# Kernel optimization log

Hardware: AMD Instinct MI355X
Metric: run time of the kernel (lower is better)

## Reference

```python
import jax, jax.numpy as jnp
import numpy as np

DIM = 768
HEADS = 12
HIDDEN = 3072
EPS = 1e-5  # torch nn.LayerNorm default


def _layer_norm(x, w, b):
    m = jnp.mean(x, axis=-1, keepdims=True)
    v = jnp.mean(jnp.square(x - m), axis=-1, keepdims=True)
    return (x - m) * jax.lax.rsqrt(v + EPS) * w + b


def setup_inputs() -> dict:
    key = jax.random.key(0)
    ks = jax.random.split(key, 10)
    s = lambda fan_in: 1.0 / np.sqrt(fan_in)
    return {
        "x": jax.random.normal(ks[0], (4, 2048, DIM), dtype=jnp.float32),
        "ln1_w": jnp.ones((DIM,), jnp.float32),
        "ln1_b": jnp.zeros((DIM,), jnp.float32),
        "qkv_w": jax.random.normal(ks[1], (3 * DIM, DIM), jnp.float32) * s(DIM),
        "qkv_b": jnp.zeros((3 * DIM,), jnp.float32),
        "proj_w": jax.random.normal(ks[2], (DIM, DIM), jnp.float32) * s(DIM),
        "proj_b": jnp.zeros((DIM,), jnp.float32),
        "ln2_w": jnp.ones((DIM,), jnp.float32),
        "ln2_b": jnp.zeros((DIM,), jnp.float32),
        "fc1_w": jax.random.normal(ks[3], (HIDDEN, DIM), jnp.float32) * s(DIM),
        "fc1_b": jnp.zeros((HIDDEN,), jnp.float32),
        "fc2_w": jax.random.normal(ks[4], (DIM, HIDDEN), jnp.float32) * s(HIDDEN),
        "fc2_b": jnp.zeros((DIM,), jnp.float32),
    }


def _attention(x, qkv_w, qkv_b, proj_w, proj_b):
    B, N, C = x.shape
    H = HEADS
    D = C // H
    scale = D ** -0.5
    qkv = x @ qkv_w.T + qkv_b                       # [B,N,3C]
    qkv = qkv.reshape(B, N, 3, H, D)
    q, k, v = jnp.moveaxis(qkv, 2, 0)               # each [B,N,H,D]
    attn = jnp.einsum("bnhd,bmhd->bhnm", q, k) * scale
    attn = jax.nn.softmax(attn, axis=-1)
    out = jnp.einsum("bhnm,bmhd->bnhd", attn, v).reshape(B, N, C)
    return out @ proj_w.T + proj_b


def reference(x, ln1_w, ln1_b, qkv_w, qkv_b, proj_w, proj_b,
              ln2_w, ln2_b, fc1_w, fc1_b, fc2_w, fc2_b):
    x = x + _attention(_layer_norm(x, ln1_w, ln1_b), qkv_w, qkv_b, proj_w, proj_b)
    h = _layer_norm(x, ln2_w, ln2_b)
    h = jax.nn.gelu(h @ fc1_w.T + fc1_b, approximate=False)
    x = x + (h @ fc2_w.T + fc2_b)
    return x
```

## Files before the change

kernel.cpp:

```cpp
#include <hip/hip_runtime.h>
#include <cstddef>


typedef _Float16 h8 __attribute__((ext_vector_type(8)));
typedef _Float16 h4 __attribute__((ext_vector_type(4)));
typedef _Float16 h2 __attribute__((ext_vector_type(2)));
typedef float f4 __attribute__((ext_vector_type(4)));

#define MFMA16(a, b, c) __builtin_amdgcn_mfma_f32_16x16x32_f16((a), (b), (c), 0, 0, 0)

__device__ __forceinline__ _Float16 f2h(float x) { return (_Float16)x; }
__device__ __forceinline__ h2 pk2(float a, float b) {
    return __builtin_bit_cast(h2, __builtin_amdgcn_cvt_pkrtz(a, b));
}
__device__ __forceinline__ h4 pk4(float a, float b, float c, float d) {
    h2 p0 = pk2(a, b);
    h2 p1 = pk2(c, d);
    h4 r; r[0] = p0[0]; r[1] = p0[1]; r[2] = p1[0]; r[3] = p1[1];
    return r;
}

__device__ __forceinline__ void gl_lds16(const _Float16* g, _Float16* l) {
    __builtin_amdgcn_global_load_lds(
        (const __attribute__((address_space(1))) void*)g,
        (__attribute__((address_space(3))) void*)l, 16, 0, 0);
}

__global__ void cvt_all(const float* __restrict__ s0, _Float16* __restrict__ d0, int n0,
                        const float* __restrict__ s1, _Float16* __restrict__ d1, int n1,
                        const float* __restrict__ s2, _Float16* __restrict__ d2, int n2,
                        const float* __restrict__ s3, _Float16* __restrict__ d3) {
    int i = (blockIdx.x * 256 + threadIdx.x) * 4;
    const float* s; _Float16* d; int base;
    if (i < n0) { s = s0; d = d0; base = 0; }
    else if (i < n0 + n1) { s = s1; d = d1; base = n0; }
    else if (i < n0 + n1 + n2) { s = s2; d = d2; base = n0 + n1; }
    else { s = s3; d = d3; base = n0 + n1 + n2; }
    int j = i - base;
    float4 v = *(const float4*)(s + j);
    *(h4*)(d + j) = pk4(v.x, v.y, v.z, v.w);
}

__global__ void ln_f16(const float* __restrict__ x, const float* __restrict__ w,
                       const float* __restrict__ b, _Float16* __restrict__ out) {
    int row = blockIdx.x;
    int tid = threadIdx.x;
    float4 v = ((const float4*)(x + (size_t)row * 768))[tid];
    float s = v.x + v.y + v.z + v.w;
    float s2 = v.x * v.x + v.y * v.y + v.z * v.z + v.w * v.w;
#pragma unroll
    for (int off = 32; off > 0; off >>= 1) {
        s += __shfl_down(s, off, 64);
        s2 += __shfl_down(s2, off, 64);
    }
    __shared__ float red[6];
    if ((tid & 63) == 0) { red[tid >> 6] = s; red[3 + (tid >> 6)] = s2; }
    __syncthreads();
    s = red[0] + red[1] + red[2];
    s2 = red[3] + red[4] + red[5];
    float mean = s * (1.0f / 768.0f);
    float rstd = rsqrtf(s2 * (1.0f / 768.0f) - mean * mean + 1e-5f);
    float4 wv = ((const float4*)w)[tid];
    float4 bv = ((const float4*)b)[tid];
    *(h4*)(out + (size_t)row * 768 + tid * 4) =
        pk4((v.x - mean) * rstd * wv.x + bv.x, (v.y - mean) * rstd * wv.y + bv.y,
            (v.z - mean) * rstd * wv.z + bv.z, (v.w - mean) * rstd * wv.w + bv.w);
}

enum { MODE_QKV = 0, MODE_PROJ = 1, MODE_FC1 = 2, MODE_FC2 = 3 };

template <int MODE, int TM>
__global__ __launch_bounds__(256, TM == 64 ? 4 : 3) void gemm_bt(
    const _Float16* __restrict__ A, const _Float16* __restrict__ W,
    const float* __restrict__ bias, const float* __restrict__ resid,
    float* __restrict__ outF, _Float16* __restrict__ oq,
    _Float16* __restrict__ okk, _Float16* __restrict__ ov, int K) {
    constexpr int MI = TM / 32;
    constexpr int AI = TM / 32;
    __shared__ _Float16 As[TM * 64];
    __shared__ _Float16 Bs[128 * 64];
    int bm = blockIdx.x * TM, bn = blockIdx.y * 128;
    int tid = threadIdx.x;
    int wave = tid >> 6, lane = tid & 63, quad = lane >> 4, l15 = lane & 15;
    int wrow = (wave >> 1) * (TM / 2), wcol = (wave & 1) * 64;
    int lr = lane >> 3;
    int sw = ((lane & 7) ^ lr) * 8;
    int rsw = (l15 & 7) * 8;
    f4 acc[MI][4];
#pragma unroll
    for (int mi = 0; mi < MI; mi++)
#pragma unroll
        for (int ni = 0; ni < 4; ni++) acc[mi][ni] = (f4){0.f, 0.f, 0.f, 0.f};

    const _Float16* ApG[AI];
    _Float16* AsL[AI];
#pragma unroll
    for (int i = 0; i < AI; i++) {
        int r = wave * (TM / 4) + i * 8;
        ApG[i] = A + (size_t)(bm + r + lr) * K + sw;
        AsL[i] = As + r * 64;
    }
    const _Float16* WpG[4];
    _Float16* BsL[4];
#pragma unroll
    for (int i = 0; i < 4; i++) {
        int r = wave * 32 + i * 8;
        WpG[i] = W + (size_t)(bn + r + lr) * K + sw;
        BsL[i] = Bs + r * 64;
    }

    for (int k0 = 0; k0 < K; k0 += 64) {
        __syncthreads();
#pragma unroll
        for (int i = 0; i < AI; i++) { gl_lds16(ApG[i], AsL[i]); ApG[i] += 64; }
#pragma unroll
        for (int i = 0; i < 4; i++) { gl_lds16(WpG[i], BsL[i]); WpG[i] += 64; }
        __syncthreads();
#pragma unroll
        for (int ks = 0; ks < 2; ks++) {
            h8 af[MI], bfr[4];
#pragma unroll
            for (int mi = 0; mi < MI; mi++)
                af[mi] = *(const h8*)&As[(wrow + 16 * mi + l15) * 64 +
                                         (((4 * ks + quad) * 8) ^ rsw)];
#pragma unroll
            for (int ni = 0; ni < 4; ni++)
                bfr[ni] = *(const h8*)&Bs[(wcol + 16 * ni + l15) * 64 +
                                          (((4 * ks + quad) * 8) ^ rsw)];
#pragma unroll
            for (int mi = 0; mi < MI; mi++)
#pragma unroll
                for (int ni = 0; ni < 4; ni++)
                    acc[mi][ni] = MFMA16(af[mi], bfr[ni], acc[mi][ni]);
        }
    }

#pragma unroll
    for (int mi = 0; mi < MI; mi++) {
#pragma unroll
        for (int ni = 0; ni < 4; ni++) {
            int col = bn + wcol + 16 * ni + l15;
            float bc = bias[col];
            int m0 = bm + wrow + 16 * mi + quad * 4;
            float v0 = acc[mi][ni][0] + bc, v1 = acc[mi][ni][1] + bc;
            float v2 = acc[mi][ni][2] + bc, v3 = acc[mi][ni][3] + bc;
            if (MODE == MODE_QKV) {
                int sec = col / 768;
                int rem = col - sec * 768;
                int h = rem >> 6, d = rem & 63;
                int b_ = m0 >> 11, ns = m0 & 2047;
                size_t bh = (size_t)(b_ * 12 + h);
                if (sec == 0) {
                    size_t base = (bh * 2048 + ns) * 64 + d;
                    oq[base] = f2h(v0 * 0.18033688f);
                    oq[base + 64] = f2h(v1 * 0.18033688f);
                    oq[base + 128] = f2h(v2 * 0.18033688f);
                    oq[base + 192] = f2h(v3 * 0.18033688f);
                } else if (sec == 1) {
                    size_t base = (bh * 2048 + ns) * 64 + d;
                    okk[base] = f2h(v0);
                    okk[base + 64] = f2h(v1);
                    okk[base + 128] = f2h(v2);
                    okk[base + 192] = f2h(v3);
                } else {
                    *(h4*)&ov[(bh * 64 + d) * 2048 + ns] = pk4(v0, v1, v2, v3);
                }
            } else if (MODE == MODE_FC1) {
                float g0 = __expf(v0 * (1.5957691f + 0.14295405f * v0 * v0));
                float g1 = __expf(v1 * (1.5957691f + 0.14295405f * v1 * v1));
                float g2 = __expf(v2 * (1.5957691f + 0.14295405f * v2 * v2));
                float g3 = __expf(v3 * (1.5957691f + 0.14295405f * v3 * v3));
                size_t base = (size_t)m0 * 3072 + col;
                oq[base] = f2h(v0 * g0 / (1.f + g0));
                oq[base + 3072] = f2h(v1 * g1 / (1.f + g1));
                oq[base + 6144] = f2h(v2 * g2 / (1.f + g2));
                oq[base + 9216] = f2h(v3 * g3 / (1.f + g3));
            } else {
                size_t idx = (size_t)m0 * 768 + col;
                outF[idx] = v0 + resid[idx];
                outF[idx + 768] = v1 + resid[idx + 768];
                outF[idx + 1536] = v2 + resid[idx + 1536];
                outF[idx + 2304] = v3 + resid[idx + 2304];
            }
        }
    }
}

__global__ __launch_bounds__(256, 4) void attn_kernel(
    const _Float16* __restrict__ Q, const _Float16* __restrict__ Kp,
    const _Float16* __restrict__ Vt, _Float16* __restrict__ O0p,
    _Float16* __restrict__ O1p, float* __restrict__ Lp) {
    int qt = blockIdx.x;
    int bh = blockIdx.y;
    int sp = blockIdx.z;
    int tid = threadIdx.x;
    int wave = tid >> 6, lane = tid & 63, quad = lane >> 4, l15 = lane & 15;
    int lr = lane >> 3;
    int sw = ((lane & 7) ^ lr) * 8;
    int rsw = (l15 & 7) * 8;

    __shared__ _Float16 Ks[64 * 64];
    __shared__ _Float16 Vs[64 * 64];
    __shared__ _Float16 Ps[4][32 * 64];

    h8 qf[2][2];
    {
        const _Float16* Qb =
            Q + (((size_t)bh * 2048) + qt * 128 + wave * 32 + l15) * 64 + quad * 8;
#pragma unroll
        for (int qc = 0; qc < 2; qc++)
#pragma unroll
            for (int ks = 0; ks < 2; ks++)
                qf[qc][ks] = *(const h8*)(Qb + qc * 16 * 64 + ks * 32);
    }
    h8 onesv;
#pragma unroll
    for (int j = 0; j < 8; j++) onesv[j] = (_Float16)1.0f;

    f4 Oa[4][2];
    f4 Ls[2];
#pragma unroll
    for (int dc = 0; dc < 4; dc++)
#pragma unroll
        for (int qc = 0; qc < 2; qc++) Oa[dc][qc] = (f4){0.f, 0.f, 0.f, 0.f};
    Ls[0] = (f4){0.f, 0.f, 0.f, 0.f};
    Ls[1] = (f4){0.f, 0.f, 0.f, 0.f};

    const _Float16* Kg = Kp + (size_t)bh * 2048 * 64;
    const _Float16* Vg = Vt + (size_t)bh * 64 * 2048;
    const _Float16* KpG[2];
    const _Float16* VpG[2];
    _Float16* KsL[2];
    _Float16* VsL[2];
#pragma unroll
    for (int i = 0; i < 2; i++) {
        int r = wave * 16 + i * 8;
        KpG[i] = Kg + (size_t)(sp * 1024 + r + lr) * 64 + sw;
        VpG[i] = Vg + (size_t)(r + lr) * 2048 + sp * 1024 + sw;
        KsL[i] = Ks + r * 64;
        VsL[i] = Vs + r * 64;
    }
    _Float16* PsW = Ps[wave];

    for (int it = 0; it < 16; it++) {
        __syncthreads();
#pragma unroll
        for (int i = 0; i < 2; i++) {
            gl_lds16(KpG[i], KsL[i]); KpG[i] += 4096;
            gl_lds16(VpG[i], VsL[i]); VpG[i] += 64;
        }
        __syncthreads();

        f4 Sa[4][2];
#pragma unroll
        for (int kc = 0; kc < 4; kc++)
#pragma unroll
            for (int qc = 0; qc < 2; qc++) Sa[kc][qc] = (f4){0.f, 0.f, 0.f, 0.f};
#pragma unroll
        for (int ks = 0; ks < 2; ks++) {
            h8 kf[4];
#pragma unroll
            for (int kc = 0; kc < 4; kc++)
                kf[kc] = *(const h8*)&Ks[(16 * kc + l15) * 64 +
                                         (((4 * ks + quad) * 8) ^ rsw)];
#pragma unroll
            for (int kc = 0; kc < 4; kc++)
#pragma unroll
                for (int qc = 0; qc < 2; qc++)
                    Sa[kc][qc] = MFMA16(kf[kc], qf[qc][ks], Sa[kc][qc]);
        }

#pragma unroll
        for (int kc = 0; kc < 4; kc++) {
#pragma unroll
            for (int qc = 0; qc < 2; qc++) {
                h4 p = pk4(exp2f(Sa[kc][qc][0]), exp2f(Sa[kc][qc][1]),
                           exp2f(Sa[kc][qc][2]), exp2f(Sa[kc][qc][3]));
                *(h4*)&PsW[(16 * qc + l15) * 64 + (((2 * kc + (quad >> 1)) * 8) ^ rsw) +
                           (quad & 1) * 4] = p;
            }
        }

#pragma unroll
        for (int ks = 0; ks < 2; ks++) {
            h8 vf[4], pf[2];
#pragma unroll
            for (int dc = 0; dc < 4; dc++)
                vf[dc] = *(const h8*)&Vs[(16 * dc + l15) * 64 +
                                         (((4 * ks + quad) * 8) ^ rsw)];
#pragma unroll
            for (int qc = 0; qc < 2; qc++)
                pf[qc] = *(const h8*)&PsW[(16 * qc + l15) * 64 +
                                          (((4 * ks + quad) * 8) ^ rsw)];
#pragma unroll
            for (int dc = 0; dc < 4; dc++)
#pragma unroll
                for (int qc = 0; qc < 2; qc++)
                    Oa[dc][qc] = MFMA16(vf[dc], pf[qc], Oa[dc][qc]);
#pragma unroll
            for (int qc = 0; qc < 2; qc++)
                Ls[qc] = MFMA16(onesv, pf[qc], Ls[qc]);
        }
    }

    _Float16* Op = (sp == 0 ? O0p : O1p);
#pragma unroll
    for (int qc = 0; qc < 2; qc++) {
        int n = qt * 128 + wave * 32 + 16 * qc + l15;
        size_t rbase = ((size_t)bh * 2048 + n) * 64;
#pragma unroll
        for (int dc = 0; dc < 4; dc++) {
            f4 o = Oa[dc][qc];
            *(h4*)&Op[rbase + 16 * dc + quad * 4] =
                pk4(o[0] * 0.015625f, o[1] * 0.015625f, o[2] * 0.015625f, o[3] * 0.015625f);
        }
        if (quad == 0) Lp[(size_t)sp * 98304 + (size_t)bh * 2048 + n] = Ls[qc][0];
    }
}

__global__ void attn_combine(const _Float16* __restrict__ O0p,
                             const _Float16* __restrict__ O1p,
                             const float* __restrict__ Lp,
                             _Float16* __restrict__ O) {
    int gid = blockIdx.x * 256 + threadIdx.x;
    int idx = gid >> 4;
    int dg = (gid & 15) * 4;
    int bh = idx >> 11, n = idx & 2047;
    size_t pbase = (size_t)idx * 64 + dg;
    h4 a = *(const h4*)&O0p[pbase];
    h4 b = *(const h4*)&O1p[pbase];
    float inv = 64.0f / (Lp[idx] + Lp[98304 + idx]);
    int b_ = bh / 12, h = bh - b_ * 12;
    *(h4*)&O[((size_t)b_ * 2048 + n) * 768 + h * 64 + dg] =
        pk4(((float)a[0] + (float)b[0]) * inv, ((float)a[1] + (float)b[1]) * inv,
            ((float)a[2] + (float)b[2]) * inv, ((float)a[3] + (float)b[3]) * inv);
}

extern "C" void kernel_launch(void* const* d_in, const int* in_sizes, int n_in,
                              void* d_out, int out_size, void* d_ws, size_t ws_size,
                              hipStream_t stream) {
    const float* x      = (const float*)d_in[0];
    const float* ln1_w  = (const float*)d_in[1];
    const float* ln1_b  = (const float*)d_in[2];
    const float* qkv_w  = (const float*)d_in[3];
    const float* qkv_b  = (const float*)d_in[4];
    const float* proj_w = (const float*)d_in[5];
    const float* proj_b = (const float*)d_in[6];
    const float* ln2_w  = (const float*)d_in[7];
    const float* ln2_b  = (const float*)d_in[8];
    const float* fc1_w  = (const float*)d_in[9];
    const float* fc1_b  = (const float*)d_in[10];
    const float* fc2_w  = (const float*)d_in[11];
    const float* fc2_b  = (const float*)d_in[12];
    float* out = (float*)d_out;

    char* ws = (char*)d_ws;
    size_t off = 0;
    _Float16* wqkv  = (_Float16*)(ws + off); off += (size_t)2304 * 768 * 2;
    _Float16* wproj = (_Float16*)(ws + off); off += (size_t)768 * 768 * 2;
    _Float16* wfc1  = (_Float16*)(ws + off); off += (size_t)3072 * 768 * 2;
    _Float16* wfc2  = (_Float16*)(ws + off); off += (size_t)768 * 3072 * 2;
    _Float16* actA  = (_Float16*)(ws + off); off += (size_t)8192 * 768 * 2;
    _Float16* big   = (_Float16*)(ws + off); off += (size_t)8192 * 3072 * 2;
    _Float16* O0p   = (_Float16*)(ws + off); off += (size_t)48 * 2048 * 64 * 2;
    float*    Lp    = (float*)(ws + off);    off += (size_t)2 * 48 * 2048 * 4;
    _Float16* qb = big;
    _Float16* kb = big + (size_t)48 * 2048 * 64;
    _Float16* vb = big + (size_t)2 * 48 * 2048 * 64;
    _Float16* O1p = big + (size_t)3 * 48 * 2048 * 64;
    _Float16* hb = big;

    cvt_all<<<6912, 256, 0, stream>>>(qkv_w, wqkv, 2304 * 768, proj_w, wproj, 768 * 768,
                                      fc1_w, wfc1, 3072 * 768, fc2_w, wfc2);

    ln_f16<<<8192, 192, 0, stream>>>(x, ln1_w, ln1_b, actA);
    gemm_bt<MODE_QKV, 128><<<dim3(64, 18), 256, 0, stream>>>(actA, wqkv, qkv_b, nullptr,
                                                             nullptr, qb, kb, vb, 768);
    attn_kernel<<<dim3(16, 48, 2), 256, 0, stream>>>(qb, kb, vb, O0p, O1p, Lp);
    attn_combine<<<6144, 256, 0, stream>>>(O0p, O1p, Lp, actA);
    gemm_bt<MODE_PROJ, 64><<<dim3(128, 6), 256, 0, stream>>>(actA, wproj, proj_b, x, out,
                                                             nullptr, nullptr, nullptr, 768);
    ln_f16<<<8192, 192, 0, stream>>>(out, ln2_w, ln2_b, actA);
    gemm_bt<MODE_FC1, 128><<<dim3(64, 24), 256, 0, stream>>>(actA, wfc1, fc1_b, nullptr,
                                                             nullptr, hb, nullptr, nullptr, 768);
    gemm_bt<MODE_FC2, 64><<<dim3(128, 6), 256, 0, stream>>>(hb, wfc2, fc2_b, out, out,
                                                            nullptr, nullptr, nullptr, 3072);
}
```

Measured before the change: 382.6 us.

## Double-buffer GEMM and attention LDS tiles, drop attention split-K combine

Makes the GEMM and attention kernels double-buffer their LDS tiles, so the next K/V or A/W tile is fetched while the current one is consumed, and removes one barrier per iteration. All GEMMs now use 64-row tiles. The attention kernel no longer splits the key range in two: each block walks all 32 key tiles, normalizes by its own row sum, and writes straight into the [B,N,C] layout, which removes the combine kernel and its partial buffers. The cost is more LDS per block, lower occupancy (launch bounds drop to 3) and fewer attention blocks in flight.

```diff
diff --git a/kernel.cpp b/kernel.cpp
--- a/kernel.cpp
+++ b/kernel.cpp
@@ -69,66 +69,70 @@
 
 enum { MODE_QKV = 0, MODE_PROJ = 1, MODE_FC1 = 2, MODE_FC2 = 3 };
 
-template <int MODE, int TM>
-__global__ __launch_bounds__(256, TM == 64 ? 4 : 3) void gemm_bt(
+template <int MODE>
+__global__ __launch_bounds__(256, 3) void gemm_bt(
     const _Float16* __restrict__ A, const _Float16* __restrict__ W,
     const float* __restrict__ bias, const float* __restrict__ resid,
     float* __restrict__ outF, _Float16* __restrict__ oq,
     _Float16* __restrict__ okk, _Float16* __restrict__ ov, int K) {
-    constexpr int MI = TM / 32;
-    constexpr int AI = TM / 32;
-    __shared__ _Float16 As[TM * 64];
-    __shared__ _Float16 Bs[128 * 64];
-    int bm = blockIdx.x * TM, bn = blockIdx.y * 128;
+    __shared__ _Float16 As[2 * 64 * 64];
+    __shared__ _Float16 Bs[2 * 128 * 64];
+    int bm = blockIdx.x * 64, bn = blockIdx.y * 128;
     int tid = threadIdx.x;
     int wave = tid >> 6, lane = tid & 63, quad = lane >> 4, l15 = lane & 15;
-    int wrow = (wave >> 1) * (TM / 2), wcol = (wave & 1) * 64;
+    int wrow = (wave >> 1) * 32, wcol = (wave & 1) * 64;
     int lr = lane >> 3;
     int sw = ((lane & 7) ^ lr) * 8;
     int rsw = (l15 & 7) * 8;
-    f4 acc[MI][4];
-#pragma unroll
-    for (int mi = 0; mi < MI; mi++)
+    f4 acc[2][4];
+#pragma unroll
+    for (int mi = 0; mi < 2; mi++)
 #pragma unroll
         for (int ni = 0; ni < 4; ni++) acc[mi][ni] = (f4){0.f, 0.f, 0.f, 0.f};
 
-    const _Float16* ApG[AI];
-    _Float16* AsL[AI];
-#pragma unroll
-    for (int i = 0; i < AI; i++) {
-        int r = wave * (TM / 4) + i * 8;
-        ApG[i] = A + (size_t)(bm + r + lr) * K + sw;
-        AsL[i] = As + r * 64;
+    const _Float16* ApG[2];
+    int rA[2];
+#pragma unroll
+    for (int i = 0; i < 2; i++) {
+        rA[i] = wave * 16 + i * 8;
+        ApG[i] = A + (size_t)(bm + rA[i] + lr) * K + sw;
     }
     const _Float16* WpG[4];
-    _Float16* BsL[4];
+    int rB[4];
 #pragma unroll
     for (int i = 0; i < 4; i++) {
-        int r = wave * 32 + i * 8;
-        WpG[i] = W + (size_t)(bn + r + lr) * K + sw;
-        BsL[i] = Bs + r * 64;
-    }
-
-    for (int k0 = 0; k0 < K; k0 += 64) {
+        rB[i] = wave * 32 + i * 8;
+        WpG[i] = W + (size_t)(bn + rB[i] + lr) * K + sw;
+    }
+
+#pragma unroll
+    for (int i = 0; i < 2; i++) { gl_lds16(ApG[i], As + rA[i] * 64); ApG[i] += 64; }
+#pragma unroll
+    for (int i = 0; i < 4; i++) { gl_lds16(WpG[i], Bs + rB[i] * 64); WpG[i] += 64; }
+
+    int nIter = K >> 6;
+    for (int it = 0; it < nIter; it++) {
+        int bufA = (it & 1) * 4096, bufN = ((it & 1) ^ 1) * 4096;
         __syncthreads();
-#pragma unroll
-        for (int i = 0; i < AI; i++) { gl_lds16(ApG[i], AsL[i]); ApG[i] += 64; }
-#pragma unroll
-        for (int i = 0; i < 4; i++) { gl_lds16(WpG[i], BsL[i]); WpG[i] += 64; }
-        __syncthreads();
+        if (it + 1 < nIter) {
+#pragma unroll
+            for (int i = 0; i < 2; i++) { gl_lds16(ApG[i], As + bufN + rA[i] * 64); ApG[i] += 64; }
+#pragma unroll
+            for (int i = 0; i < 4; i++) { gl_lds16(WpG[i], Bs + 2 * bufN + rB[i] * 64); WpG[i] += 64; }
+        }
 #pragma unroll
         for (int ks = 0; ks < 2; ks++) {
-            h8 af[MI], bfr[4];
-#pragma unroll
-            for (int mi = 0; mi < MI; mi++)
-                af[mi] = *(const h8*)&As[(wrow + 16 * mi + l15) * 64 +
+            h8 af[2], bfr[4];
+#pragma unroll
+            for (int mi = 0; mi < 2; mi++)
+                af[mi] = *(const h8*)&As[bufA + (wrow + 16 * mi + l15) * 64 +
                                          (((4 * ks + quad) * 8) ^ rsw)];
 #pragma unroll
             for (int ni = 0; ni < 4; ni++)
-                bfr[ni] = *(const h8*)&Bs[(wcol + 16 * ni + l15) * 64 +
+                bfr[ni] = *(const h8*)&Bs[2 * bufA + (wcol + 16 * ni + l15) * 64 +
                                           (((4 * ks + quad) * 8) ^ rsw)];
 #pragma unroll
-            for (int mi = 0; mi < MI; mi++)
+            for (int mi = 0; mi < 2; mi++)
 #pragma unroll
                 for (int ni = 0; ni < 4; ni++)
                     acc[mi][ni] = MFMA16(af[mi], bfr[ni], acc[mi][ni]);
@@ -136,7 +140,7 @@
     }
 
 #pragma unroll
-    for (int mi = 0; mi < MI; mi++) {
+    for (int mi = 0; mi < 2; mi++) {
 #pragma unroll
         for (int ni = 0; ni < 4; ni++) {
             int col = bn + wcol + 16 * ni + l15;
@@ -186,21 +190,19 @@
     }
 }
 
-__global__ __launch_bounds__(256, 4) void attn_kernel(
+__global__ __launch_bounds__(256, 3) void attn_kernel(
     const _Float16* __restrict__ Q, const _Float16* __restrict__ Kp,
-    const _Float16* __restrict__ Vt, _Float16* __restrict__ O0p,
-    _Float16* __restrict__ O1p, float* __restrict__ Lp) {
-    int qt = blockIdx.x;
-    int bh = blockIdx.y;
-    int sp = blockIdx.z;
+    const _Float16* __restrict__ Vt, _Float16* __restrict__ O) {
+    int bh = blockIdx.x;
+    int qt = blockIdx.y;
     int tid = threadIdx.x;
     int wave = tid >> 6, lane = tid & 63, quad = lane >> 4, l15 = lane & 15;
     int lr = lane >> 3;
     int sw = ((lane & 7) ^ lr) * 8;
     int rsw = (l15 & 7) * 8;
 
-    __shared__ _Float16 Ks[64 * 64];
-    __shared__ _Float16 Vs[64 * 64];
+    __shared__ _Float16 Ks[2 * 64 * 64];
+    __shared__ _Float16 Vs[2 * 64 * 64];
     __shared__ _Float16 Ps[4][32 * 64];
 
     h8 qf[2][2];
@@ -230,26 +232,31 @@
     const _Float16* Vg = Vt + (size_t)bh * 64 * 2048;
     const _Float16* KpG[2];
     const _Float16* VpG[2];
-    _Float16* KsL[2];
-    _Float16* VsL[2];
+    int rKV[2];
 #pragma unroll
     for (int i = 0; i < 2; i++) {
-        int r = wave * 16 + i * 8;
-        KpG[i] = Kg + (size_t)(sp * 1024 + r + lr) * 64 + sw;
-        VpG[i] = Vg + (size_t)(r + lr) * 2048 + sp * 1024 + sw;
-        KsL[i] = Ks + r * 64;
-        VsL[i] = Vs + r * 64;
+        rKV[i] = wave * 16 + i * 8;
+        KpG[i] = Kg + (size_t)(rKV[i] + lr) * 64 + sw;
+        VpG[i] = Vg + (size_t)(rKV[i] + lr) * 2048 + sw;
     }
     _Float16* PsW = Ps[wave];
 
-    for (int it = 0; it < 16; it++) {
+#pragma unroll
+    for (int i = 0; i < 2; i++) {
+        gl_lds16(KpG[i], Ks + rKV[i] * 64); KpG[i] += 4096;
+        gl_lds16(VpG[i], Vs + rKV[i] * 64); VpG[i] += 64;
+    }
+
+    for (int it = 0; it < 32; it++) {
+        int bufC = (it & 1) * 4096, bufN = ((it & 1) ^ 1) * 4096;
         __syncthreads();
-#pragma unroll
-        for (int i = 0; i < 2; i++) {
-            gl_lds16(KpG[i], KsL[i]); KpG[i] += 4096;
-            gl_lds16(VpG[i], VsL[i]); VpG[i] += 64;
-        }
-        __syncthreads();
+        if (it + 1 < 32) {
+#pragma unroll
+            for (int i = 0; i < 2; i++) {
+                gl_lds16(KpG[i], Ks + bufN + rKV[i] * 64); KpG[i] += 4096;
+                gl_lds16(VpG[i], Vs + bufN + rKV[i] * 64); VpG[i] += 64;
+            }
+        }
 
         f4 Sa[4][2];
 #pragma unroll
@@ -261,7 +268,7 @@
             h8 kf[4];
 #pragma unroll
             for (int kc = 0; kc < 4; kc++)
-                kf[kc] = *(const h8*)&Ks[(16 * kc + l15) * 64 +
+                kf[kc] = *(const h8*)&Ks[bufC + (16 * kc + l15) * 64 +
                                          (((4 * ks + quad) * 8) ^ rsw)];
 #pragma unroll
             for (int kc = 0; kc < 4; kc++)
@@ -286,7 +293,7 @@
             h8 vf[4], pf[2];
 #pragma unroll
             for (int dc = 0; dc < 4; dc++)
-                vf[dc] = *(const h8*)&Vs[(16 * dc + l15) * 64 +
+                vf[dc] = *(const h8*)&Vs[bufC + (16 * dc + l15) * 64 +
                                          (((4 * ks + quad) * 8) ^ rsw)];
 #pragma unroll
             for (int qc = 0; qc < 2; qc++)
@@ -303,37 +310,19 @@
         }
     }
 
-    _Float16* Op = (sp == 0 ? O0p : O1p);
+    int b_ = bh / 12, h = bh - b_ * 12;
 #pragma unroll
     for (int qc = 0; qc < 2; qc++) {
+        float inv = 1.0f / Ls[qc][0];
         int n = qt * 128 + wave * 32 + 16 * qc + l15;
-        size_t rbase = ((size_t)bh * 2048 + n) * 64;
+        size_t base = ((size_t)b_ * 2048 + n) * 768 + h * 64;
 #pragma unroll
         for (int dc = 0; dc < 4; dc++) {
             f4 o = Oa[dc][qc];
-            *(h4*)&Op[rbase + 16 * dc + quad * 4] =
-                pk4(o[0] * 0.015625f, o[1] * 0.015625f, o[2] * 0.015625f, o[3] * 0.015625f);
-        }
-        if (quad == 0) Lp[(size_t)sp * 98304 + (size_t)bh * 2048 + n] = Ls[qc][0];
-    }
-}
-
-__global__ void attn_combine(const _Float16* __restrict__ O0p,
-                             const _Float16* __restrict__ O1p,
-                             const float* __restrict__ Lp,
-                             _Float16* __restrict__ O) {
-    int gid = blockIdx.x * 256 + threadIdx.x;
-    int idx = gid >> 4;
-    int dg = (gid & 15) * 4;
-    int bh = idx >> 11, n = idx & 2047;
-    size_t pbase = (size_t)idx * 64 + dg;
-    h4 a = *(const h4*)&O0p[pbase];
-    h4 b = *(const h4*)&O1p[pbase];
-    float inv = 64.0f / (Lp[idx] + Lp[98304 + idx]);
-    int b_ = bh / 12, h = bh - b_ * 12;
-    *(h4*)&O[((size_t)b_ * 2048 + n) * 768 + h * 64 + dg] =
-        pk4(((float)a[0] + (float)b[0]) * inv, ((float)a[1] + (float)b[1]) * inv,
-            ((float)a[2] + (float)b[2]) * inv, ((float)a[3] + (float)b[3]) * inv);
+            *(h4*)&O[base + 16 * dc + quad * 4] =
+                pk4(o[0] * inv, o[1] * inv, o[2] * inv, o[3] * inv);
+        }
+    }
 }
 
 extern "C" void kernel_launch(void* const* d_in, const int* in_sizes, int n_in,
@@ -362,27 +351,23 @@
     _Float16* wfc2  = (_Float16*)(ws + off); off += (size_t)768 * 3072 * 2;
     _Float16* actA  = (_Float16*)(ws + off); off += (size_t)8192 * 768 * 2;
     _Float16* big   = (_Float16*)(ws + off); off += (size_t)8192 * 3072 * 2;
-    _Float16* O0p   = (_Float16*)(ws + off); off += (size_t)48 * 2048 * 64 * 2;
-    float*    Lp    = (float*)(ws + off);    off += (size_t)2 * 48 * 2048 * 4;
     _Float16* qb = big;
     _Float16* kb = big + (size_t)48 * 2048 * 64;
     _Float16* vb = big + (size_t)2 * 48 * 2048 * 64;
-    _Float16* O1p = big + (size_t)3 * 48 * 2048 * 64;
     _Float16* hb = big;
 
     cvt_all<<<6912, 256, 0, stream>>>(qkv_w, wqkv, 2304 * 768, proj_w, wproj, 768 * 768,
                                       fc1_w, wfc1, 3072 * 768, fc2_w, wfc2);
 
     ln_f16<<<8192, 192, 0, stream>>>(x, ln1_w, ln1_b, actA);
-    gemm_bt<MODE_QKV, 128><<<dim3(64, 18), 256, 0, stream>>>(actA, wqkv, qkv_b, nullptr,
-                                                             nullptr, qb, kb, vb, 768);
-    attn_kernel<<<dim3(16, 48, 2), 256, 0, stream>>>(qb, kb, vb, O0p, O1p, Lp);
-    attn_combine<<<6144, 256, 0, stream>>>(O0p, O1p, Lp, actA);
-    gemm_bt<MODE_PROJ, 64><<<dim3(128, 6), 256, 0, stream>>>(actA, wproj, proj_b, x, out,
-                                                             nullptr, nullptr, nullptr, 768);
+    gemm_bt<MODE_QKV><<<dim3(128, 18), 256, 0, stream>>>(actA, wqkv, qkv_b, nullptr,
+                                                         nullptr, qb, kb, vb, 768);
+    attn_kernel<<<dim3(48, 16), 256, 0, stream>>>(qb, kb, vb, actA);
+    gemm_bt<MODE_PROJ><<<dim3(128, 6), 256, 0, stream>>>(actA, wproj, proj_b, x, out,
+                                                         nullptr, nullptr, nullptr, 768);
     ln_f16<<<8192, 192, 0, stream>>>(out, ln2_w, ln2_b, actA);
-    gemm_bt<MODE_FC1, 128><<<dim3(64, 24), 256, 0, stream>>>(actA, wfc1, fc1_b, nullptr,
-                                                             nullptr, hb, nullptr, nullptr, 768);
-    gemm_bt<MODE_FC2, 64><<<dim3(128, 6), 256, 0, stream>>>(hb, wfc2, fc2_b, out, out,
-                                                            nullptr, nullptr, nullptr, 3072);
-}
+    gemm_bt<MODE_FC1><<<dim3(128, 24), 256, 0, stream>>>(actA, wfc1, fc1_b, nullptr,
+                                                         nullptr, hb, nullptr, nullptr, 768);
+    gemm_bt<MODE_FC2><<<dim3(128, 6), 256, 0, stream>>>(hb, wfc2, fc2_b, out, out,
+                                                        nullptr, nullptr, nullptr, 3072);
+}
```

After: 379.5 us. Within noise of the previous version (-0.8%).

## Drop attention split-K, double-buffer K/V tiles, keep P in registers

Applied to the files above, without the earlier changes.

The attention kernel no longer splits the key range across two blocks. Each block now walks all 32 K/V tiles and normalizes its output directly, so the combine kernel and the partial-output buffers go away. K/V loads are double-buffered so the next tile's global-to-LDS copy overlaps compute, removing one barrier per iteration. The P matrix stays in registers and feeds 16x16x16 MFMAs instead of round-tripping through LDS. In exchange the grid has half as many blocks, the K=16 MFMAs are narrower, and the launch bound drops to 3 blocks per SM.

```diff
diff --git a/kernel.cpp b/kernel.cpp
--- a/kernel.cpp
+++ b/kernel.cpp
@@ -8,6 +8,7 @@
 typedef float f4 __attribute__((ext_vector_type(4)));
 
 #define MFMA16(a, b, c) __builtin_amdgcn_mfma_f32_16x16x32_f16((a), (b), (c), 0, 0, 0)
+#define MFMAK16(a, b, c) __builtin_amdgcn_mfma_f32_16x16x16f16((a), (b), (c), 0, 0, 0)
 
 __device__ __forceinline__ _Float16 f2h(float x) { return (_Float16)x; }
 __device__ __forceinline__ h2 pk2(float a, float b) {
@@ -186,22 +187,19 @@
     }
 }
 
-__global__ __launch_bounds__(256, 4) void attn_kernel(
+__global__ __launch_bounds__(256, 3) void attn_kernel(
     const _Float16* __restrict__ Q, const _Float16* __restrict__ Kp,
-    const _Float16* __restrict__ Vt, _Float16* __restrict__ O0p,
-    _Float16* __restrict__ O1p, float* __restrict__ Lp) {
-    int qt = blockIdx.x;
-    int bh = blockIdx.y;
-    int sp = blockIdx.z;
+    const _Float16* __restrict__ Vt, _Float16* __restrict__ O) {
+    int bh = blockIdx.x;
+    int qt = blockIdx.y;
     int tid = threadIdx.x;
     int wave = tid >> 6, lane = tid & 63, quad = lane >> 4, l15 = lane & 15;
     int lr = lane >> 3;
     int sw = ((lane & 7) ^ lr) * 8;
     int rsw = (l15 & 7) * 8;
 
-    __shared__ _Float16 Ks[64 * 64];
-    __shared__ _Float16 Vs[64 * 64];
-    __shared__ _Float16 Ps[4][32 * 64];
+    __shared__ _Float16 Ks[2 * 64 * 64];
+    __shared__ _Float16 Vs[2 * 64 * 64];
 
     h8 qf[2][2];
     {
@@ -213,9 +211,9 @@
             for (int ks = 0; ks < 2; ks++)
                 qf[qc][ks] = *(const h8*)(Qb + qc * 16 * 64 + ks * 32);
     }
-    h8 onesv;
-#pragma unroll
-    for (int j = 0; j < 8; j++) onesv[j] = (_Float16)1.0f;
+    h4 ones4;
+#pragma unroll
+    for (int j = 0; j < 4; j++) ones4[j] = (_Float16)1.0f;
 
     f4 Oa[4][2];
     f4 Ls[2];
@@ -230,26 +228,30 @@
     const _Float16* Vg = Vt + (size_t)bh * 64 * 2048;
     const _Float16* KpG[2];
     const _Float16* VpG[2];
-    _Float16* KsL[2];
-    _Float16* VsL[2];
+    int rKV[2];
 #pragma unroll
     for (int i = 0; i < 2; i++) {
-        int r = wave * 16 + i * 8;
-        KpG[i] = Kg + (size_t)(sp * 1024 + r + lr) * 64 + sw;
-        VpG[i] = Vg + (size_t)(r + lr) * 2048 + sp * 1024 + sw;
-        KsL[i] = Ks + r * 64;
-        VsL[i] = Vs + r * 64;
-    }
-    _Float16* PsW = Ps[wave];
-
-    for (int it = 0; it < 16; it++) {
+        rKV[i] = wave * 16 + i * 8;
+        KpG[i] = Kg + (size_t)(rKV[i] + lr) * 64 + sw;
+        VpG[i] = Vg + (size_t)(rKV[i] + lr) * 2048 + sw;
+    }
+
+#pragma unroll
+    for (int i = 0; i < 2; i++) {
+        gl_lds16(KpG[i], Ks + rKV[i] * 64); KpG[i] += 4096;
+        gl_lds16(VpG[i], Vs + rKV[i] * 64); VpG[i] += 64;
+    }
+
+    for (int it = 0; it < 32; it++) {
+        int bufC = (it & 1) * 4096, bufN = ((it & 1) ^ 1) * 4096;
         __syncthreads();
-#pragma unroll
-        for (int i = 0; i < 2; i++) {
-            gl_lds16(KpG[i], KsL[i]); KpG[i] += 4096;
-            gl_lds16(VpG[i], VsL[i]); VpG[i] += 64;
-        }
-        __syncthreads();
+        if (it + 1 < 32) {
+#pragma unroll
+            for (int i = 0; i < 2; i++) {
+                gl_lds16(KpG[i], Ks + bufN + rKV[i] * 64); KpG[i] += 4096;
+                gl_lds16(VpG[i], Vs + bufN + rKV[i] * 64); VpG[i] += 64;
+            }
+        }
 
         f4 Sa[4][2];
 #pragma unroll
@@ -261,7 +263,7 @@
             h8 kf[4];
 #pragma unroll
             for (int kc = 0; kc < 4; kc++)
-                kf[kc] = *(const h8*)&Ks[(16 * kc + l15) * 64 +
+                kf[kc] = *(const h8*)&Ks[bufC + (16 * kc + l15) * 64 +
                                          (((4 * ks + quad) * 8) ^ rsw)];
 #pragma unroll
             for (int kc = 0; kc < 4; kc++)
@@ -270,70 +272,46 @@
                     Sa[kc][qc] = MFMA16(kf[kc], qf[qc][ks], Sa[kc][qc]);
         }
 
+        h4 p[4][2];
+#pragma unroll
+        for (int kc = 0; kc < 4; kc++)
+#pragma unroll
+            for (int qc = 0; qc < 2; qc++)
+                p[kc][qc] = pk4(exp2f(Sa[kc][qc][0]), exp2f(Sa[kc][qc][1]),
+                                exp2f(Sa[kc][qc][2]), exp2f(Sa[kc][qc][3]));
+
 #pragma unroll
         for (int kc = 0; kc < 4; kc++) {
-#pragma unroll
-            for (int qc = 0; qc < 2; qc++) {
-                h4 p = pk4(exp2f(Sa[kc][qc][0]), exp2f(Sa[kc][qc][1]),
-                           exp2f(Sa[kc][qc][2]), exp2f(Sa[kc][qc][3]));
-                *(h4*)&PsW[(16 * qc + l15) * 64 + (((2 * kc + (quad >> 1)) * 8) ^ rsw) +
-                           (quad & 1) * 4] = p;
-            }
-        }
-
-#pragma unroll
-        for (int ks = 0; ks < 2; ks++) {
-            h8 vf[4], pf[2];
+            h4 vf4[4];
 #pragma unroll
             for (int dc = 0; dc < 4; dc++)
-                vf[dc] = *(const h8*)&Vs[(16 * dc + l15) * 64 +
-                                         (((4 * ks + quad) * 8) ^ rsw)];
+                vf4[dc] = *(const h4*)&Vs[bufC + (16 * dc + l15) * 64 +
+                                          (((2 * kc + (quad >> 1)) * 8) ^ rsw) +
+                                          (quad & 1) * 4];
+#pragma unroll
+            for (int dc = 0; dc < 4; dc++)
+#pragma unroll
+                for (int qc = 0; qc < 2; qc++)
+                    Oa[dc][qc] = MFMAK16(vf4[dc], p[kc][qc], Oa[dc][qc]);
 #pragma unroll
             for (int qc = 0; qc < 2; qc++)
-                pf[qc] = *(const h8*)&PsW[(16 * qc + l15) * 64 +
-                                          (((4 * ks + quad) * 8) ^ rsw)];
-#pragma unroll
-            for (int dc = 0; dc < 4; dc++)
-#pragma unroll
-                for (int qc = 0; qc < 2; qc++)
-                    Oa[dc][qc] = MFMA16(vf[dc], pf[qc], Oa[dc][qc]);
-#pragma unroll
-            for (int qc = 0; qc < 2; qc++)
-                Ls[qc] = MFMA16(onesv, pf[qc], Ls[qc]);
-        }
-    }
-
-    _Float16* Op = (sp == 0 ? O0p : O1p);
+                Ls[qc] = MFMAK16(ones4, p[kc][qc], Ls[qc]);
+        }
+    }
+
+    int b_ = bh / 12, h = bh - b_ * 12;
 #pragma unroll
     for (int qc = 0; qc < 2; qc++) {
+        float inv = 1.0f / Ls[qc][0];
         int n = qt * 128 + wave * 32 + 16 * qc + l15;
-        size_t rbase = ((size_t)bh * 2048 + n) * 64;
+        size_t base = ((size_t)b_ * 2048 + n) * 768 + h * 64;
 #pragma unroll
         for (int dc = 0; dc < 4; dc++) {
             f4 o = Oa[dc][qc];
-            *(h4*)&Op[rbase + 16 * dc + quad * 4] =
-                pk4(o[0] * 0.015625f, o[1] * 0.015625f, o[2] * 0.015625f, o[3] * 0.015625f);
-        }
-        if (quad == 0) Lp[(size_t)sp * 98304 + (size_t)bh * 2048 + n] = Ls[qc][0];
-    }
-}
-
-__global__ void attn_combine(const _Float16* __restrict__ O0p,
-                             const _Float16* __restrict__ O1p,
-                             const float* __restrict__ Lp,
-                             _Float16* __restrict__ O) {
-    int gid = blockIdx.x * 256 + threadIdx.x;
-    int idx = gid >> 4;
-    int dg = (gid & 15) * 4;
-    int bh = idx >> 11, n = idx & 2047;
-    size_t pbase = (size_t)idx * 64 + dg;
-    h4 a = *(const h4*)&O0p[pbase];
-    h4 b = *(const h4*)&O1p[pbase];
-    float inv = 64.0f / (Lp[idx] + Lp[98304 + idx]);
-    int b_ = bh / 12, h = bh - b_ * 12;
-    *(h4*)&O[((size_t)b_ * 2048 + n) * 768 + h * 64 + dg] =
-        pk4(((float)a[0] + (float)b[0]) * inv, ((float)a[1] + (float)b[1]) * inv,
-            ((float)a[2] + (float)b[2]) * inv, ((float)a[3] + (float)b[3]) * inv);
+            *(h4*)&O[base + 16 * dc + quad * 4] =
+                pk4(o[0] * inv, o[1] * inv, o[2] * inv, o[3] * inv);
+        }
+    }
 }
 
 extern "C" void kernel_launch(void* const* d_in, const int* in_sizes, int n_in,
@@ -362,12 +340,9 @@
     _Float16* wfc2  = (_Float16*)(ws + off); off += (size_t)768 * 3072 * 2;
     _Float16* actA  = (_Float16*)(ws + off); off += (size_t)8192 * 768 * 2;
     _Float16* big   = (_Float16*)(ws + off); off += (size_t)8192 * 3072 * 2;
-    _Float16* O0p   = (_Float16*)(ws + off); off += (size_t)48 * 2048 * 64 * 2;
-    float*    Lp    = (float*)(ws + off);    off += (size_t)2 * 48 * 2048 * 4;
     _Float16* qb = big;
     _Float16* kb = big + (size_t)48 * 2048 * 64;
     _Float16* vb = big + (size_t)2 * 48 * 2048 * 64;
-    _Float16* O1p = big + (size_t)3 * 48 * 2048 * 64;
     _Float16* hb = big;
 
     cvt_all<<<6912, 256, 0, stream>>>(qkv_w, wqkv, 2304 * 768, proj_w, wproj, 768 * 768,
@@ -376,8 +351,7 @@
     ln_f16<<<8192, 192, 0, stream>>>(x, ln1_w, ln1_b, actA);
     gemm_bt<MODE_QKV, 128><<<dim3(64, 18), 256, 0, stream>>>(actA, wqkv, qkv_b, nullptr,
                                                              nullptr, qb, kb, vb, 768);
-    attn_kernel<<<dim3(16, 48, 2), 256, 0, stream>>>(qb, kb, vb, O0p, O1p, Lp);
-    attn_combine<<<6144, 256, 0, stream>>>(O0p, O1p, Lp, actA);
+    attn_kernel<<<dim3(48, 16), 256, 0, stream>>>(qb, kb, vb, actA);
     gemm_bt<MODE_PROJ, 64><<<dim3(128, 6), 256, 0, stream>>>(actA, wproj, proj_b, x, out,
                                                              nullptr, nullptr, nullptr, 768);
     ln_f16<<<8192, 192, 0, stream>>>(out, ln2_w, ln2_b, actA);
```

New measurement: 370.6 us. 3.1% less time.
